# Kernel tuning notes

Hardware: AMD Instinct MI355X
Metric: run time of the kernel (lower is better)

## Reference

```python
import jax, jax.numpy as jnp
import numpy as np

N_QUBITS = 21
N_LAYERS = 3
BATCH = 4


def _ry(state, w, theta, n):
    # Apply RY(theta) on wire w. state: (B, 2**n) real float32.
    # RY = [[cos(t/2), -sin(t/2)], [sin(t/2), cos(t/2)]] (real matrix).
    B = state.shape[0]
    s = state.reshape(B, 2 ** w, 2, 2 ** (n - w - 1))
    c = jnp.cos(theta / 2).reshape(-1, 1, 1)   # (B,1,1) or (1,1,1)
    sn = jnp.sin(theta / 2).reshape(-1, 1, 1)
    a0 = s[:, :, 0, :]
    a1 = s[:, :, 1, :]
    out = jnp.stack([c * a0 - sn * a1, sn * a0 + c * a1], axis=2)
    return out.reshape(B, -1)


def _cnot(state, c, t, n):
    # CNOT(control=c, target=t): flip target axis on the control=1 subspace.
    B = state.shape[0]
    lo, hi = (c, t) if c < t else (t, c)
    s = state.reshape(B, 2 ** lo, 2, 2 ** (hi - lo - 1), 2, 2 ** (n - hi - 1))
    ca, ta = (2, 4) if c == lo else (4, 2)
    c0 = jax.lax.index_in_dim(s, 0, axis=ca, keepdims=True)
    c1 = jnp.flip(jax.lax.index_in_dim(s, 1, axis=ca, keepdims=True), axis=ta)
    return jnp.concatenate([c0, c1], axis=ca).reshape(B, -1)


def setup_inputs() -> dict:
    key = jax.random.key(0)
    k1, k2 = jax.random.split(key)
    x = jax.random.normal(k1, (BATCH, N_QUBITS), dtype=jnp.float32)
    # TorchLayer default init: uniform in [0, 2*pi)
    weights = jax.random.uniform(k2, (N_LAYERS, N_QUBITS), dtype=jnp.float32) * (2.0 * np.pi)
    return {"x": x, "weights": weights}


def reference(x, weights):
    B, n = x.shape
    L = weights.shape[0]
    # |0...0> initial state; circuit is entirely real (RY, CNOT), so float32.
    state = jnp.zeros((B, 2 ** n), dtype=x.dtype).at[:, 0].set(1.0)
    # Input encoding: RY(x_i) on each wire.
    for i in range(n):
        state = _ry(state, i, x[:, i], n)
    # Variational layers: ring CNOTs then RY(weights[j, i]).
    for j in range(L):
        for i in range(n):
            state = _cnot(state, i, (i + 1) % n, n)
        for i in range(n):
            state = _ry(state, i, weights[j, i], n)
    # <Z_i> = P(bit_i = 0) - P(bit_i = 1)
    probs = state * state
    z = []
    for i in range(n):
        p = probs.reshape(B, 2 ** i, 2, -1).sum(axis=(1, 3))  # (B, 2)
        z.append(p[:, 0] - p[:, 1])
    return jnp.stack(z, axis=1)  # (B, n_qubits)
```

## Files before the change

### kernel.cpp

```cpp
#include <hip/hip_runtime.h>
#include <hip/hip_fp16.h>


#define NQ 21
#define SW(a) ((a) ^ (((a) >> 3) & 7))
#define SHC(q) __shfl(cv, (q)), __shfl(sv, (q))

template<int Q>
__device__ __forceinline__ void ry32(float* v, float c, float s) {
#pragma unroll
  for (int k = 0; k < 16; ++k) {
    int l0 = ((k >> Q) << (Q + 1)) | (k & ((1 << Q) - 1));
    int l1 = l0 | (1 << Q);
    float a0 = v[l0], a1 = v[l1];
    v[l0] = c * a0 - s * a1;
    v[l1] = s * a0 + c * a1;
  }
}

template<int C, int T>
__device__ __forceinline__ void cnot32(float* v) {
  constexpr int lo = (C < T) ? C : T;
  constexpr int hi = (C < T) ? T : C;
#pragma unroll
  for (int k = 0; k < 8; ++k) {
    int i1 = ((k >> lo) << (lo + 1)) | (k & ((1 << lo) - 1));
    int i2 = ((i1 >> hi) << (hi + 1)) | (i1 & ((1 << hi) - 1));
    int a = i2 | (1 << C);
    int b = a | (1 << T);
    float tmp = v[a]; v[a] = v[b]; v[b] = tmp;
  }
}

__device__ __forceinline__ void ld4(const uint2* __restrict__ g, int idx, float* dst) {
  uint2 r = g[idx];
  __half2 h0 = *reinterpret_cast<__half2*>(&r.x);
  __half2 h1 = *reinterpret_cast<__half2*>(&r.y);
  float2 f0 = __half22float2(h0), f1 = __half22float2(h1);
  dst[0] = f0.x; dst[1] = f0.y; dst[2] = f1.x; dst[3] = f1.y;
}
__device__ __forceinline__ uint2 pk4(const float* src) {
  __half2 h0 = __floats2half2_rn(src[0], src[1]);
  __half2 h1 = __floats2half2_rn(src[2], src[3]);
  uint2 r;
  r.x = *reinterpret_cast<unsigned int*>(&h0);
  r.y = *reinterpret_cast<unsigned int*>(&h1);
  return r;
}

#define A1 (tid | (rr << 9))
#define A2 ((tid & 0x7F) | (rr << 7) | ((tid >> 7) << 10))
#define A3 ((tid & 0x1F) | (rr << 5) | ((tid >> 5) << 8))
#define A4 ((tid & 7) | (rr << 3) | ((tid >> 3) << 6))
#define A5 ((tid & 1) | (rr << 1) | ((tid >> 1) << 4))
#define A6 (rr | (tid << 3))
#define GH(l4) (((l4) & 0xF) | (t << 4) | (((l4) >> 4) << 11))

template<bool INIT>
__global__ __launch_bounds__(512, 4) void k_L(const float* __restrict__ x,
                                              const float* __restrict__ w,
                                              unsigned long long stp) {
  __shared__ __align__(16) float s[16384];
  float4* s4 = reinterpret_cast<float4*>(s);
  const int tid = threadIdx.x, lane = tid & 63;
  const int b = blockIdx.x >> 7, t = blockIdx.x & 127;
  float cv = 1.f, sv = 0.f;
  if (lane < NQ) sincosf(0.5f * w[lane], &sv, &cv);
  uint2* g2 = reinterpret_cast<uint2*>(stp) + ((size_t)b << 19) + ((size_t)t << 12);
  float v[32];

  if (INIT) {
    float cx = 1.f, sx = 0.f;
    if (lane < NQ) sincosf(0.5f * x[b * NQ + lane], &sx, &cx);
    float Qp = 1.f;
#pragma unroll
    for (int i = 0; i < 9; ++i) {
      float cq = __shfl(cx, 18 - i), sq = __shfl(sx, 18 - i);
      Qp *= ((tid >> i) & 1) ? sq : cq;
    }
    float hfac[2];
#pragma unroll
    for (int bb = 0; bb < 2; ++bb) {
      int h = (t << 1) | bb;
      int h0 = h ^ (h >> 1);
      float p = 1.f;
#pragma unroll
      for (int j = 0; j < 8; ++j) {
        float cq = __shfl(cx, 7 - j), sq = __shfl(sx, 7 - j);
        p *= ((h0 >> j) & 1) ? sq : cq;
      }
      hfac[bb] = p;
    }
    float c20 = __shfl(cx, 20), s20 = __shfl(sx, 20);
    float c19 = __shfl(cx, 19), s19 = __shfl(sx, 19);
    float c9  = __shfl(cx, 9),  s9  = __shfl(sx, 9);
    float c8  = __shfl(cx, 8),  s8  = __shfl(sx, 8);
    float w0t[4], w1t[4];
#pragma unroll
    for (int i = 0; i < 4; ++i) {
      w0t[i] = ((i & 1) ? s20 : c20) * ((i & 2) ? s19 : c19);
      w1t[i] = ((i & 1) ? s9  : c9 ) * ((i & 2) ? s8  : c8 );
    }
#pragma unroll
    for (int r = 0; r < 32; ++r)
      v[r] = hfac[(r >> 4) & 1] * w1t[(r >> 2) & 3] * w0t[r & 3] * Qp;
  } else {
#pragma unroll
    for (int rr = 0; rr < 8; ++rr) ld4(g2, A1, v + 4 * rr);
  }
  cnot32<4, 3>(v); cnot32<3, 2>(v);
  ry32<4>(v, SHC(7)); ry32<3>(v, SHC(8));
#pragma unroll
  for (int rr = 0; rr < 8; ++rr) s4[SW(A1)] = *reinterpret_cast<float4*>(v + 4 * rr);
  __syncthreads();

#pragma unroll
  for (int rr = 0; rr < 8; ++rr) *reinterpret_cast<float4*>(v + 4 * rr) = s4[SW(A2)];
  cnot32<4, 3>(v); cnot32<3, 2>(v);
  ry32<4>(v, SHC(9)); ry32<3>(v, SHC(10));
#pragma unroll
  for (int rr = 0; rr < 8; ++rr) s4[SW(A2)] = *reinterpret_cast<float4*>(v + 4 * rr);
  __syncthreads();

#pragma unroll
  for (int rr = 0; rr < 8; ++rr) *reinterpret_cast<float4*>(v + 4 * rr) = s4[SW(A3)];
  cnot32<4, 3>(v); cnot32<3, 2>(v);
  ry32<4>(v, SHC(11)); ry32<3>(v, SHC(12));
#pragma unroll
  for (int rr = 0; rr < 8; ++rr) s4[SW(A3)] = *reinterpret_cast<float4*>(v + 4 * rr);
  __syncthreads();

#pragma unroll
  for (int rr = 0; rr < 8; ++rr) *reinterpret_cast<float4*>(v + 4 * rr) = s4[SW(A4)];
  cnot32<4, 3>(v); cnot32<3, 2>(v);
  ry32<4>(v, SHC(13)); ry32<3>(v, SHC(14));
#pragma unroll
  for (int rr = 0; rr < 8; ++rr) s4[SW(A4)] = *reinterpret_cast<float4*>(v + 4 * rr);
  __syncthreads();

#pragma unroll
  for (int rr = 0; rr < 8; ++rr) *reinterpret_cast<float4*>(v + 4 * rr) = s4[SW(A5)];
  cnot32<4, 3>(v); cnot32<3, 2>(v);
  ry32<4>(v, SHC(15)); ry32<3>(v, SHC(16));
#pragma unroll
  for (int rr = 0; rr < 8; ++rr) s4[SW(A5)] = *reinterpret_cast<float4*>(v + 4 * rr);
  __syncthreads();

#pragma unroll
  for (int rr = 0; rr < 8; ++rr) *reinterpret_cast<float4*>(v + 4 * rr) = s4[SW(A6)];
  cnot32<3, 2>(v); cnot32<2, 1>(v); cnot32<1, 0>(v);
  ry32<3>(v, SHC(17)); ry32<2>(v, SHC(18)); ry32<1>(v, SHC(19));
  {
    uint4* g4o = reinterpret_cast<uint4*>(g2);
#pragma unroll
    for (int rr = 0; rr < 8; rr += 2) {
      uint2 lo = pk4(v + 4 * rr), hi = pk4(v + 4 * rr + 4);
      uint4 o; o.x = lo.x; o.y = lo.y; o.z = hi.x; o.w = hi.y;
      g4o[((rr | (tid << 3)) >> 1)] = o;
    }
  }
}

__global__ __launch_bounds__(512, 4) void k_H(const float* __restrict__ w,
                                              unsigned long long stp) {
  __shared__ __align__(16) float s[16384];
  float4* s4 = reinterpret_cast<float4*>(s);
  const int tid = threadIdx.x, lane = tid & 63;
  const int b = blockIdx.x >> 7, t = blockIdx.x & 127;
  float cv = 1.f, sv = 0.f;
  if (lane < NQ) sincosf(0.5f * w[lane], &sv, &cv);
  uint2* gb = reinterpret_cast<uint2*>(stp) + ((size_t)b << 19);
  float v[32];

#pragma unroll
  for (int rr = 0; rr < 8; ++rr) ld4(gb, GH(A1), v + 4 * rr);
  cnot32<0, 4>(v);
  ry32<0>(v, SHC(20)); ry32<4>(v, SHC(0)); ry32<3>(v, SHC(1)); ry32<2>(v, SHC(2));
  cnot32<4, 3>(v); cnot32<3, 2>(v);
#pragma unroll
  for (int rr = 0; rr < 8; ++rr) s4[SW(A1)] = *reinterpret_cast<float4*>(v + 4 * rr);
  __syncthreads();

#pragma unroll
  for (int rr = 0; rr < 8; ++rr) *reinterpret_cast<float4*>(v + 4 * rr) = s4[SW(A2)];
  ry32<3>(v, SHC(3)); ry32<2>(v, SHC(4));
  cnot32<4, 3>(v); cnot32<3, 2>(v);
#pragma unroll
  for (int rr = 0; rr < 8; ++rr) s4[SW(A2)] = *reinterpret_cast<float4*>(v + 4 * rr);
  __syncthreads();

#pragma unroll
  for (int rr = 0; rr < 8; ++rr) *reinterpret_cast<float4*>(v + 4 * rr) = s4[SW(A3)];
  ry32<3>(v, SHC(5)); ry32<2>(v, SHC(6));
  cnot32<4, 3>(v); cnot32<3, 2>(v);
#pragma unroll
  for (int rr = 0; rr < 8; ++rr) s4[SW(A3)] = *reinterpret_cast<float4*>(v + 4 * rr);
  __syncthreads();

#pragma unroll
  for (int rr = 0; rr < 8; ++rr) *reinterpret_cast<float4*>(v + 4 * rr) = s4[SW(A4)];
  cnot32<4, 3>(v);
#pragma unroll
  for (int rr = 0; rr < 8; ++rr) gb[GH(A4)] = pk4(v + 4 * rr);
}

__global__ __launch_bounds__(512, 4) void k_Hfin(const float* __restrict__ w,
                                                 unsigned long long stp,
                                                 float* __restrict__ partial) {
  __shared__ __align__(16) float s[16384];
  float4* s4 = reinterpret_cast<float4*>(s);
  const int tid = threadIdx.x, lane = tid & 63;
  const int b = blockIdx.x >> 7, t = blockIdx.x & 127;
  float cv = 1.f, sv = 0.f;
  if (lane < NQ) sincosf(0.5f * w[lane], &sv, &cv);
  const uint2* gb = reinterpret_cast<const uint2*>(stp) + ((size_t)b << 19);
  float v[32];

#pragma unroll
  for (int rr = 0; rr < 8; ++rr) ld4(gb, GH(A1), v + 4 * rr);
  cnot32<0, 4>(v);
  ry32<0>(v, SHC(20)); ry32<4>(v, SHC(0)); ry32<3>(v, SHC(1)); ry32<2>(v, SHC(2));
#pragma unroll
  for (int rr = 0; rr < 8; ++rr) s4[SW(A1)] = *reinterpret_cast<float4*>(v + 4 * rr);
  __syncthreads();

#pragma unroll
  for (int rr = 0; rr < 8; ++rr) *reinterpret_cast<float4*>(v + 4 * rr) = s4[SW(A2)];
  ry32<3>(v, SHC(3)); ry32<2>(v, SHC(4));
#pragma unroll
  for (int rr = 0; rr < 8; ++rr) s4[SW(A2)] = *reinterpret_cast<float4*>(v + 4 * rr);
  __syncthreads();

#pragma unroll
  for (int rr = 0; rr < 8; ++rr) *reinterpret_cast<float4*>(v + 4 * rr) = s4[SW(A3)];
  __syncthreads();
  ry32<3>(v, SHC(5)); ry32<2>(v, SHC(6));

  float S = 0, aq20 = 0, aq19 = 0, aq6 = 0, aq5 = 0, aq4 = 0;
#pragma unroll
  for (int r = 0; r < 32; ++r) {
    float p = v[r] * v[r];
    S += p;
    aq20 += (r & 1)  ? -p : p;
    aq19 += (r & 2)  ? -p : p;
    aq6  += (r & 4)  ? -p : p;
    aq5  += (r & 8)  ? -p : p;
    aq4  += (r & 16) ? -p : p;
  }
  float a21[21];
  a21[20] = aq20; a21[19] = aq19; a21[6] = aq6; a21[5] = aq5; a21[4] = aq4;
  a21[18] = (tid & 1)   ? -S : S;
  a21[17] = (tid & 2)   ? -S : S;
  a21[16] = (tid & 4)   ? -S : S;
  a21[15] = (tid & 8)   ? -S : S;
  a21[7]  = (tid & 16)  ? -S : S;
  a21[3]  = (tid & 32)  ? -S : S;
  a21[2]  = (tid & 64)  ? -S : S;
  a21[1]  = (tid & 128) ? -S : S;
  a21[0]  = (tid & 256) ? -S : S;
  a21[14] = (t & 1)  ? -S : S;
  a21[13] = (t & 2)  ? -S : S;
  a21[12] = (t & 4)  ? -S : S;
  a21[11] = (t & 8)  ? -S : S;
  a21[10] = (t & 16) ? -S : S;
  a21[9]  = (t & 32) ? -S : S;
  a21[8]  = (t & 64) ? -S : S;

  const int wv = tid >> 6;
#pragma unroll
  for (int q = 0; q < 21; ++q) {
    float val = a21[q];
    val += __shfl_down(val, 32);
    val += __shfl_down(val, 16);
    val += __shfl_down(val, 8);
    val += __shfl_down(val, 4);
    val += __shfl_down(val, 2);
    val += __shfl_down(val, 1);
    if (lane == 0) s[q * 8 + wv] = val;
  }
  __syncthreads();
  if (tid < NQ) {
    float sum = 0.f;
#pragma unroll
    for (int k = 0; k < 8; ++k) sum += s[tid * 8 + k];
    partial[blockIdx.x * NQ + tid] = sum;
  }
}

__global__ void k_red(const float* __restrict__ partial, float* __restrict__ out) {
  int tid = threadIdx.x;
  if (tid < 84) {
    int b = tid / NQ, q = tid % NQ;
    float sum = 0.f;
    for (int k = 0; k < 128; ++k) sum += partial[(b * 128 + k) * NQ + q];
    out[tid] = sum;
  }
}

extern "C" void kernel_launch(void* const* d_in, const int* in_sizes, int n_in,
                              void* d_out, int out_size, void* d_ws, size_t ws_size,
                              hipStream_t stream) {
  const float* x = (const float*)d_in[0];
  const float* w = (const float*)d_in[1];
  float* out = (float*)d_out;
  unsigned long long stp = (unsigned long long)d_ws;
  float* partial = (float*)((char*)d_ws + (((size_t)4 << 21) * 2));
  if (ws_size < ((size_t)4 << 21) * 2 + 512 * NQ * 4) return;

  dim3 grid(512), blk(512);
  k_L<true> <<<grid, blk, 0, stream>>>(x, w +  0, stp);
  k_H       <<<grid, blk, 0, stream>>>(w +  0, stp);
  k_L<false><<<grid, blk, 0, stream>>>(nullptr, w + 21, stp);
  k_H       <<<grid, blk, 0, stream>>>(w + 21, stp);
  k_L<false><<<grid, blk, 0, stream>>>(nullptr, w + 42, stp);
  k_Hfin    <<<grid, blk, 0, stream>>>(w + 42, stp, partial);
  k_red     <<<1, dim3(128), 0, stream>>>(partial, out);
}
```

Baseline: 115.5 us.

## Process four qubits per shared-memory pass with new XOR swizzle, parallelize final reduction

Each shared-memory transposition now exposes four local qubits instead of two, so k_L needs three LDS round trips instead of six and k_H/k_Hfin need fewer as well. A new swizzle function PH2 with scalar writes and float4 reads is meant to avoid bank conflicts under the new layouts. The final reduction kernel uses 672 threads with a two-level sum instead of 84 serial loops. The cost is a larger block of remapped index logic and changed qubit-to-register assignments, which could break correctness if any permutation is wrong.

```diff
diff --git a/kernel.cpp b/kernel.cpp
--- a/kernel.cpp
+++ b/kernel.cpp
@@ -3,8 +3,13 @@
 
 
 #define NQ 21
-#define SW(a) ((a) ^ (((a) >> 3) & 7))
 #define SHC(q) __shfl(cv, (q)), __shfl(sv, (q))
+
+__device__ constexpr int PH2(int slot) {
+  int blk = slot >> 2;
+  blk ^= ((blk >> 3) & 7) ^ ((blk >> 6) & 7);
+  return (blk << 2) | (slot & 3);
+}
 
 template<int Q>
 __device__ __forceinline__ void ry32(float* v, float c, float s) {
@@ -49,11 +54,6 @@
 }
 
 #define A1 (tid | (rr << 9))
-#define A2 ((tid & 0x7F) | (rr << 7) | ((tid >> 7) << 10))
-#define A3 ((tid & 0x1F) | (rr << 5) | ((tid >> 5) << 8))
-#define A4 ((tid & 7) | (rr << 3) | ((tid >> 3) << 6))
-#define A5 ((tid & 1) | (rr << 1) | ((tid >> 1) << 4))
-#define A6 (rr | (tid << 3))
 #define GH(l4) (((l4) & 0xF) | (t << 4) | (((l4) >> 4) << 11))
 
 template<bool INIT>
@@ -68,6 +68,7 @@
   if (lane < NQ) sincosf(0.5f * w[lane], &sv, &cv);
   uint2* g2 = reinterpret_cast<uint2*>(stp) + ((size_t)b << 19) + ((size_t)t << 12);
   float v[32];
+  float4* v4 = reinterpret_cast<float4*>(v);
 
   if (INIT) {
     float cx = 1.f, sx = 0.f;
@@ -110,44 +111,50 @@
   }
   cnot32<4, 3>(v); cnot32<3, 2>(v);
   ry32<4>(v, SHC(7)); ry32<3>(v, SHC(8));
-#pragma unroll
-  for (int rr = 0; rr < 8; ++rr) s4[SW(A1)] = *reinterpret_cast<float4*>(v + 4 * rr);
-  __syncthreads();
-
-#pragma unroll
-  for (int rr = 0; rr < 8; ++rr) *reinterpret_cast<float4*>(v + 4 * rr) = s4[SW(A2)];
-  cnot32<4, 3>(v); cnot32<3, 2>(v);
-  ry32<4>(v, SHC(9)); ry32<3>(v, SHC(10));
-#pragma unroll
-  for (int rr = 0; rr < 8; ++rr) s4[SW(A2)] = *reinterpret_cast<float4*>(v + 4 * rr);
-  __syncthreads();
-
-#pragma unroll
-  for (int rr = 0; rr < 8; ++rr) *reinterpret_cast<float4*>(v + 4 * rr) = s4[SW(A3)];
-  cnot32<4, 3>(v); cnot32<3, 2>(v);
-  ry32<4>(v, SHC(11)); ry32<3>(v, SHC(12));
-#pragma unroll
-  for (int rr = 0; rr < 8; ++rr) s4[SW(A3)] = *reinterpret_cast<float4*>(v + 4 * rr);
-  __syncthreads();
-
-#pragma unroll
-  for (int rr = 0; rr < 8; ++rr) *reinterpret_cast<float4*>(v + 4 * rr) = s4[SW(A4)];
-  cnot32<4, 3>(v); cnot32<3, 2>(v);
-  ry32<4>(v, SHC(13)); ry32<3>(v, SHC(14));
-#pragma unroll
-  for (int rr = 0; rr < 8; ++rr) s4[SW(A4)] = *reinterpret_cast<float4*>(v + 4 * rr);
-  __syncthreads();
-
-#pragma unroll
-  for (int rr = 0; rr < 8; ++rr) *reinterpret_cast<float4*>(v + 4 * rr) = s4[SW(A5)];
-  cnot32<4, 3>(v); cnot32<3, 2>(v);
-  ry32<4>(v, SHC(15)); ry32<3>(v, SHC(16));
-#pragma unroll
-  for (int rr = 0; rr < 8; ++rr) s4[SW(A5)] = *reinterpret_cast<float4*>(v + 4 * rr);
-  __syncthreads();
-
-#pragma unroll
-  for (int rr = 0; rr < 8; ++rr) *reinterpret_cast<float4*>(v + 4 * rr) = s4[SW(A6)];
+  {
+    const int pb = PH2(((tid & 31) << 2) | ((tid >> 5) & 3) | (((tid >> 7) & 3) << 9));
+#pragma unroll
+    for (int r = 0; r < 32; ++r)
+      s[pb ^ PH2(((r & 3) << 7) | ((r >> 2) << 11))] = v[r];
+  }
+  __syncthreads();
+
+  {
+    const int pb = PH2(((tid & 3) << 7) | (tid & 0x7C) | ((tid >> 7) << 12));
+#pragma unroll
+    for (int rr = 0; rr < 8; ++rr) v4[rr] = s4[(pb ^ PH2(rr << 9)) >> 2];
+  }
+  cnot32<4, 3>(v); cnot32<3, 2>(v); cnot32<2, 1>(v); cnot32<1, 0>(v);
+  ry32<4>(v, SHC(9)); ry32<3>(v, SHC(10)); ry32<2>(v, SHC(11)); ry32<1>(v, SHC(12));
+  __syncthreads();
+  {
+    const int pb = PH2(((tid >> 3) & 3) | (tid & 4) | ((tid & 3) << 3) |
+                       (tid & 0x60) | ((tid >> 7) << 12));
+#pragma unroll
+    for (int r = 0; r < 32; ++r) s[pb ^ PH2(r << 7)] = v[r];
+  }
+  __syncthreads();
+
+  {
+    const int pb = PH2(((tid & 3) << 3) | (tid & 4) | ((tid >> 3) << 8));
+#pragma unroll
+    for (int rr = 0; rr < 8; ++rr) v4[rr] = s4[(pb ^ PH2(rr << 5)) >> 2];
+  }
+  cnot32<4, 3>(v); cnot32<3, 2>(v); cnot32<2, 1>(v); cnot32<1, 0>(v);
+  ry32<4>(v, SHC(13)); ry32<3>(v, SHC(14)); ry32<2>(v, SHC(15)); ry32<1>(v, SHC(16));
+  __syncthreads();
+  {
+    const int pb = PH2((tid & 7) | ((tid >> 3) << 8));
+#pragma unroll
+    for (int r = 0; r < 32; ++r) s[pb ^ PH2(r << 3)] = v[r];
+  }
+  __syncthreads();
+
+  {
+    const int pb = PH2(tid << 5);
+#pragma unroll
+    for (int rr = 0; rr < 8; ++rr) v4[rr] = s4[(pb ^ PH2(rr << 2)) >> 2];
+  }
   cnot32<3, 2>(v); cnot32<2, 1>(v); cnot32<1, 0>(v);
   ry32<3>(v, SHC(17)); ry32<2>(v, SHC(18)); ry32<1>(v, SHC(19));
   {
@@ -171,37 +178,47 @@
   if (lane < NQ) sincosf(0.5f * w[lane], &sv, &cv);
   uint2* gb = reinterpret_cast<uint2*>(stp) + ((size_t)b << 19);
   float v[32];
+  float4* v4 = reinterpret_cast<float4*>(v);
 
 #pragma unroll
   for (int rr = 0; rr < 8; ++rr) ld4(gb, GH(A1), v + 4 * rr);
   cnot32<0, 4>(v);
   ry32<0>(v, SHC(20)); ry32<4>(v, SHC(0)); ry32<3>(v, SHC(1)); ry32<2>(v, SHC(2));
   cnot32<4, 3>(v); cnot32<3, 2>(v);
-#pragma unroll
-  for (int rr = 0; rr < 8; ++rr) s4[SW(A1)] = *reinterpret_cast<float4*>(v + 4 * rr);
-  __syncthreads();
-
-#pragma unroll
-  for (int rr = 0; rr < 8; ++rr) *reinterpret_cast<float4*>(v + 4 * rr) = s4[SW(A2)];
-  ry32<3>(v, SHC(3)); ry32<2>(v, SHC(4));
-  cnot32<4, 3>(v); cnot32<3, 2>(v);
-#pragma unroll
-  for (int rr = 0; rr < 8; ++rr) s4[SW(A2)] = *reinterpret_cast<float4*>(v + 4 * rr);
-  __syncthreads();
-
-#pragma unroll
-  for (int rr = 0; rr < 8; ++rr) *reinterpret_cast<float4*>(v + 4 * rr) = s4[SW(A3)];
-  ry32<3>(v, SHC(5)); ry32<2>(v, SHC(6));
-  cnot32<4, 3>(v); cnot32<3, 2>(v);
-#pragma unroll
-  for (int rr = 0; rr < 8; ++rr) s4[SW(A3)] = *reinterpret_cast<float4*>(v + 4 * rr);
-  __syncthreads();
-
-#pragma unroll
-  for (int rr = 0; rr < 8; ++rr) *reinterpret_cast<float4*>(v + 4 * rr) = s4[SW(A4)];
+  {
+    const int pb = PH2(((tid & 31) << 2) | ((tid >> 5) & 3) | (((tid >> 7) & 3) << 9));
+#pragma unroll
+    for (int r = 0; r < 32; ++r)
+      s[pb ^ PH2(((r & 3) << 7) | ((r >> 2) << 11))] = v[r];
+  }
+  __syncthreads();
+
+  {
+    const int pb = PH2(((tid & 3) << 7) | (tid & 0x7C) | ((tid >> 7) << 12));
+#pragma unroll
+    for (int rr = 0; rr < 8; ++rr) v4[rr] = s4[(pb ^ PH2(rr << 9)) >> 2];
+  }
+  ry32<3>(v, SHC(3)); ry32<2>(v, SHC(4)); ry32<1>(v, SHC(5)); ry32<0>(v, SHC(6));
+  cnot32<4, 3>(v); cnot32<3, 2>(v); cnot32<2, 1>(v); cnot32<1, 0>(v);
+  __syncthreads();
+  {
+    const int pb = PH2((tid & 127) | ((tid >> 7) << 12));
+#pragma unroll
+    for (int r = 0; r < 32; ++r) s[pb ^ PH2(r << 7)] = v[r];
+  }
+  __syncthreads();
+
+  {
+    const int pb = PH2(((tid & 7) << 2) | ((tid >> 3) << 8));
+#pragma unroll
+    for (int rr = 0; rr < 8; ++rr) v4[rr] = s4[(pb ^ PH2(rr << 5)) >> 2];
+  }
   cnot32<4, 3>(v);
 #pragma unroll
-  for (int rr = 0; rr < 8; ++rr) gb[GH(A4)] = pk4(v + 4 * rr);
+  for (int rr = 0; rr < 8; ++rr) {
+    int l4 = (tid & 7) | (rr << 3) | ((tid >> 3) << 6);
+    gb[GH(l4)] = pk4(v + 4 * rr);
+  }
 }
 
 __global__ __launch_bounds__(512, 4) void k_Hfin(const float* __restrict__ w,
@@ -215,47 +232,48 @@
   if (lane < NQ) sincosf(0.5f * w[lane], &sv, &cv);
   const uint2* gb = reinterpret_cast<const uint2*>(stp) + ((size_t)b << 19);
   float v[32];
+  float4* v4 = reinterpret_cast<float4*>(v);
 
 #pragma unroll
   for (int rr = 0; rr < 8; ++rr) ld4(gb, GH(A1), v + 4 * rr);
   cnot32<0, 4>(v);
   ry32<0>(v, SHC(20)); ry32<4>(v, SHC(0)); ry32<3>(v, SHC(1)); ry32<2>(v, SHC(2));
-#pragma unroll
-  for (int rr = 0; rr < 8; ++rr) s4[SW(A1)] = *reinterpret_cast<float4*>(v + 4 * rr);
-  __syncthreads();
-
-#pragma unroll
-  for (int rr = 0; rr < 8; ++rr) *reinterpret_cast<float4*>(v + 4 * rr) = s4[SW(A2)];
-  ry32<3>(v, SHC(3)); ry32<2>(v, SHC(4));
-#pragma unroll
-  for (int rr = 0; rr < 8; ++rr) s4[SW(A2)] = *reinterpret_cast<float4*>(v + 4 * rr);
-  __syncthreads();
-
-#pragma unroll
-  for (int rr = 0; rr < 8; ++rr) *reinterpret_cast<float4*>(v + 4 * rr) = s4[SW(A3)];
-  __syncthreads();
-  ry32<3>(v, SHC(5)); ry32<2>(v, SHC(6));
-
-  float S = 0, aq20 = 0, aq19 = 0, aq6 = 0, aq5 = 0, aq4 = 0;
+  {
+    const int pb = PH2(((tid & 31) << 2) | ((tid >> 5) & 3) | (((tid >> 7) & 3) << 9));
+#pragma unroll
+    for (int r = 0; r < 32; ++r)
+      s[pb ^ PH2(((r & 3) << 7) | ((r >> 2) << 11))] = v[r];
+  }
+  __syncthreads();
+
+  {
+    const int pb = PH2(((tid & 3) << 7) | (tid & 0x7C) | ((tid >> 7) << 12));
+#pragma unroll
+    for (int rr = 0; rr < 8; ++rr) v4[rr] = s4[(pb ^ PH2(rr << 9)) >> 2];
+  }
+  __syncthreads();
+  ry32<3>(v, SHC(3)); ry32<2>(v, SHC(4)); ry32<1>(v, SHC(5)); ry32<0>(v, SHC(6));
+
+  float S = 0, aq6 = 0, aq5 = 0, aq4 = 0, aq3 = 0, aq2 = 0;
 #pragma unroll
   for (int r = 0; r < 32; ++r) {
     float p = v[r] * v[r];
     S += p;
-    aq20 += (r & 1)  ? -p : p;
-    aq19 += (r & 2)  ? -p : p;
-    aq6  += (r & 4)  ? -p : p;
-    aq5  += (r & 8)  ? -p : p;
-    aq4  += (r & 16) ? -p : p;
+    aq6 += (r & 1)  ? -p : p;
+    aq5 += (r & 2)  ? -p : p;
+    aq4 += (r & 4)  ? -p : p;
+    aq3 += (r & 8)  ? -p : p;
+    aq2 += (r & 16) ? -p : p;
   }
   float a21[21];
-  a21[20] = aq20; a21[19] = aq19; a21[6] = aq6; a21[5] = aq5; a21[4] = aq4;
-  a21[18] = (tid & 1)   ? -S : S;
-  a21[17] = (tid & 2)   ? -S : S;
-  a21[16] = (tid & 4)   ? -S : S;
-  a21[15] = (tid & 8)   ? -S : S;
-  a21[7]  = (tid & 16)  ? -S : S;
-  a21[3]  = (tid & 32)  ? -S : S;
-  a21[2]  = (tid & 64)  ? -S : S;
+  a21[6] = aq6; a21[5] = aq5; a21[4] = aq4; a21[3] = aq3; a21[2] = aq2;
+  a21[20] = (tid & 1)   ? -S : S;
+  a21[19] = (tid & 2)   ? -S : S;
+  a21[18] = (tid & 4)   ? -S : S;
+  a21[17] = (tid & 8)   ? -S : S;
+  a21[16] = (tid & 16)  ? -S : S;
+  a21[15] = (tid & 32)  ? -S : S;
+  a21[7]  = (tid & 64)  ? -S : S;
   a21[1]  = (tid & 128) ? -S : S;
   a21[0]  = (tid & 256) ? -S : S;
   a21[14] = (t & 1)  ? -S : S;
@@ -288,11 +306,21 @@
 }
 
 __global__ void k_red(const float* __restrict__ partial, float* __restrict__ out) {
-  int tid = threadIdx.x;
+  __shared__ float red[84][8];
+  const int tid = threadIdx.x;
+  const int pair = tid >> 3, k8 = tid & 7;
+  if (pair < 84) {
+    int b = pair / NQ, q = pair % NQ;
+    float sum = 0.f;
+#pragma unroll
+    for (int i = 0; i < 16; ++i) sum += partial[(b * 128 + k8 * 16 + i) * NQ + q];
+    red[pair][k8] = sum;
+  }
+  __syncthreads();
   if (tid < 84) {
-    int b = tid / NQ, q = tid % NQ;
     float sum = 0.f;
-    for (int k = 0; k < 128; ++k) sum += partial[(b * 128 + k) * NQ + q];
+#pragma unroll
+    for (int k = 0; k < 8; ++k) sum += red[tid][k];
     out[tid] = sum;
   }
 }
@@ -314,5 +342,5 @@
   k_H       <<<grid, blk, 0, stream>>>(w + 21, stp);
   k_L<false><<<grid, blk, 0, stream>>>(nullptr, w + 42, stp);
   k_Hfin    <<<grid, blk, 0, stream>>>(w + 42, stp, partial);
-  k_red     <<<1, dim3(128), 0, stream>>>(partial, out);
-}
+  k_red     <<<1, dim3(672), 0, stream>>>(partial, out);
+}
```

Result: faster. 110.8 us (-4.0%).
